# Kernel tuning notes

Measured on AMD Instinct MI355X. Metric: run time of the kernel, lower is better.

## Reference

```python
import jax, jax.numpy as jnp
import numpy as np

N = 40000      # nodes
E = 640000     # edges (avg degree 16)
F = 128        # in_feats
OUT = 128      # out_feats


def setup_inputs() -> dict:
    key = jax.random.key(0)
    ks = jax.random.split(key, 8)
    feat = jax.random.normal(ks[0], (N, F), dtype=jnp.float32)
    src = jax.random.randint(ks[1], (E,), 0, N, dtype=jnp.int32)
    dst = jnp.sort(jax.random.randint(ks[2], (E,), 0, N, dtype=jnp.int32))
    # AttentionAGG: fc1 (2F -> F), fc2 (F -> 1); fc_layer (2F -> OUT)
    s1 = 1.0 / np.sqrt(2 * F)
    s2 = 1.0 / np.sqrt(F)
    w1 = jax.random.normal(ks[3], (2 * F, F), dtype=jnp.float32) * s1
    b1 = jnp.zeros((F,), dtype=jnp.float32)
    w2 = jax.random.normal(ks[4], (F, 1), dtype=jnp.float32) * s2
    b2 = jnp.zeros((1,), dtype=jnp.float32)
    wf = jax.random.normal(ks[5], (2 * F, OUT), dtype=jnp.float32) * s1
    bf = jnp.zeros((OUT,), dtype=jnp.float32)
    return {"feat": feat, "src": src, "dst": dst,
            "w1": w1, "b1": b1, "w2": w2, "b2": b2, "wf": wf, "bf": bf}


def reference(feat, src, dst, w1, b1, w2, b2, wf, bf):
    f = feat.shape[1]
    n = feat.shape[0]
    # fc1(concat(h_dst, m_src)) == h_dst @ w1[:F] + h_src @ w1[F:]  (edge_weight is None)
    proj_dst = feat @ w1[:f]          # [N, F]
    proj_src = feat @ w1[f:]          # [N, F]
    pre = jnp.tanh(proj_dst[dst] + proj_src[src] + b1)   # [E, F]
    scores = (pre @ w2)[:, 0] + b2[0]                    # [E]
    # softmax over the ragged incoming-edge set of each dst node
    smax = jax.ops.segment_max(scores, dst, num_segments=n, indices_are_sorted=True)
    ex = jnp.exp(scores - jax.lax.stop_gradient(smax)[dst])
    den = jax.ops.segment_sum(ex, dst, num_segments=n, indices_are_sorted=True)
    att = ex / den[dst]                                  # [E]
    # weighted segment-sum of messages (m_e = feat[src]); zero-degree nodes get 0
    neigh = jax.ops.segment_sum(att[:, None] * feat[src], dst,
                                num_segments=n, indices_are_sorted=True)  # [N, F]
    # fc_layer(concat(h_self, neigh))
    rst = feat @ wf[:f] + neigh @ wf[f:] + bf            # [N, OUT]
    return rst
```

## Files before the change

### kernel.cpp

```cpp
#include <hip/hip_runtime.h>
#include <math.h>

#define F 128
#define OUT 128

typedef unsigned short ushort_t;
typedef __attribute__((ext_vector_type(8))) short bfrag;
typedef __attribute__((ext_vector_type(4))) float ffrag;

__device__ __forceinline__ float bf_lo(unsigned int u) {
    return __uint_as_float(u << 16);
}
__device__ __forceinline__ float bf_hi(unsigned int u) {
    return __uint_as_float(u & 0xffff0000u);
}
__device__ __forceinline__ ushort_t f2bf(float f) {
    unsigned int x = __float_as_uint(f);
    unsigned int r = x + 0x7fffu + ((x >> 16) & 1u);
    return (ushort_t)(r >> 16);
}
__device__ __forceinline__ unsigned pk2(float lo, float hi) {
    return (unsigned)f2bf(lo) | ((unsigned)f2bf(hi) << 16);
}

#define DPP_ADD(x, ctrl) \
    ((x) + __int_as_float(__builtin_amdgcn_update_dpp( \
        0, __float_as_int(x), (ctrl), 0xf, 0xf, true)))

__global__ __launch_bounds__(256) void prep_kernel(
    const float* __restrict__ feat, const float* __restrict__ w1,
    const float* __restrict__ wf, const int* __restrict__ dst,
    ushort_t* __restrict__ abig, ushort_t* __restrict__ srcpack,
    ushort_t* __restrict__ btp, ushort_t* __restrict__ btf,
    int* __restrict__ row_ptr, int n, int e, int nb0, int nb1, int nb2)
{
    const int b = blockIdx.x, t = threadIdx.x;
    if (b < nb0) {
        int i = b * 256 + t;
        if (i >= n * 16) return;
        int row = i >> 4, c = (i & 15) * 8;
        float4 a = *(const float4*)(feat + (size_t)row * F + c);
        float4 bb = *(const float4*)(feat + (size_t)row * F + c + 4);
        unsigned p0 = pk2(a.x, a.y), p1 = pk2(a.z, a.w);
        unsigned p2 = pk2(bb.x, bb.y), p3 = pk2(bb.z, bb.w);
        *(uint4*)(abig + (size_t)row * 256 + c) = make_uint4(p0, p1, p2, p3);
        *(uint2*)(srcpack + (size_t)row * 256 + c * 2 + 4) = make_uint2(p0, p1);
        *(uint2*)(srcpack + (size_t)row * 256 + c * 2 + 12) = make_uint2(p2, p3);
    } else if (b < nb0 + nb1) {
        int idx = (b - nb0) * 256 + t;
        int j = idx >> 7, k = idx & 127;
        float v = (j < F) ? w1[(size_t)k * F + j]
                          : w1[(size_t)(F + k) * F + (j - F)];
        btp[idx] = f2bf(v);
    } else if (b < nb0 + nb1 + nb2) {
        int idx = (b - nb0 - nb1) * 256 + t;
        int j = idx >> 8, k = idx & 255;
        btf[idx] = f2bf(wf[(size_t)k * F + j]);
    } else {
        int i = (b - nb0 - nb1 - nb2) * 256 + t;
        if (i >= e) return;
        int d = dst[i];
        int prev = (i == 0) ? -1 : dst[i - 1];
        for (int v = prev + 1; v <= d; ++v) row_ptr[v] = i;
        if (i == e - 1) {
            for (int v = d + 1; v <= n; ++v) row_ptr[v] = e;
        }
    }
}

#define PST 136
__global__ __launch_bounds__(256) void proj_gemm_kernel(
    const ushort_t* __restrict__ abig, const ushort_t* __restrict__ btp,
    const float* __restrict__ b1, ushort_t* __restrict__ e_dst,
    ushort_t* __restrict__ srcpack, int n)
{
    __shared__ ushort_t As[64 * PST];
    __shared__ ushort_t Ep[4][16 * 80];
    const int t = threadIdx.x;
    const int wv = t >> 6, lane = t & 63;
    const int lm = lane & 15, quad = lane >> 4;
    const int row0 = blockIdx.x * 64, col0 = wv * 64;

#pragma unroll
    for (int k = 0; k < 4; ++k) {
        int l = k * 256 + t;
        int r = l >> 4, ch = l & 15;
        uint4 d = make_uint4(0, 0, 0, 0);
        if (row0 + r < n) d = *(const uint4*)(abig + (size_t)(row0 + r) * 256 + ch * 8);
        *(uint4*)(As + r * PST + ch * 8) = d;
    }
    __syncthreads();

    bfrag bfr[4][4];
#pragma unroll
    for (int ks = 0; ks < 4; ++ks)
#pragma unroll
        for (int ni = 0; ni < 4; ++ni)
            bfr[ks][ni] = *(const bfrag*)(btp + (size_t)(col0 + ni * 16 + lm) * 128
                                          + ks * 32 + quad * 8);

    ffrag acc[4][4];
#pragma unroll
    for (int mi = 0; mi < 4; ++mi)
#pragma unroll
        for (int ni = 0; ni < 4; ++ni) acc[mi][ni] = (ffrag){0.f, 0.f, 0.f, 0.f};

#pragma unroll
    for (int ks = 0; ks < 4; ++ks)
#pragma unroll
        for (int mi = 0; mi < 4; ++mi) {
            bfrag af = *(const bfrag*)(As + (mi * 16 + lm) * PST + ks * 32 + quad * 8);
#pragma unroll
            for (int ni = 0; ni < 4; ++ni)
                acc[mi][ni] = __builtin_amdgcn_mfma_f32_16x16x32_bf16(
                    af, bfr[ks][ni], acc[mi][ni], 0, 0, 0);
        }

    float bias[4];
#pragma unroll
    for (int ni = 0; ni < 4; ++ni)
        bias[ni] = (col0 < F) ? b1[col0 + ni * 16 + lm] : 0.f;

#pragma unroll
    for (int mi = 0; mi < 4; ++mi) {
#pragma unroll
        for (int ni = 0; ni < 4; ++ni)
#pragma unroll
            for (int r = 0; r < 4; ++r)
                Ep[wv][(quad * 4 + r) * 80 + ni * 16 + lm] =
                    f2bf(__expf(2.f * (acc[mi][ni][r] + bias[ni])));
#pragma unroll
        for (int ps = 0; ps < 2; ++ps) {
            int rl = ps * 8 + (lane >> 3), co = (lane & 7) * 8;
            uint4 vv = *(const uint4*)(&Ep[wv][rl * 80 + co]);
            int grow = row0 + mi * 16 + rl;
            if (grow < n) {
                if (col0 < F) {
                    *(uint4*)(e_dst + (size_t)grow * F + col0 + co) = vv;
                } else {
                    int f0 = col0 - F + co;
                    *(uint2*)(srcpack + (size_t)grow * 256 + f0 * 2) =
                        make_uint2(vv.x, vv.y);
                    *(uint2*)(srcpack + (size_t)grow * 256 + f0 * 2 + 8) =
                        make_uint2(vv.z, vv.w);
                }
            }
        }
    }
}

__global__ __launch_bounds__(256) void fused_kernel(
    const ushort_t* __restrict__ e_dst, const ushort_t* __restrict__ srcpack,
    const int* __restrict__ src, const int* __restrict__ row_ptr,
    const float* __restrict__ w2, ushort_t* __restrict__ abig, int n, int nhw)
{
    const int hw0 = (int)((blockIdx.x * 256u + threadIdx.x) >> 5);
    const int fl = threadIdx.x & 31;

    const float4 wv4 = ((const float4*)w2)[fl];
    const float w0 = wv4.x, w1_ = wv4.y, w2_ = wv4.z, w3_ = wv4.w;
    float sw = w0 + w1_ + w2_ + w3_;
    float aw = fabsf(w0) + fabsf(w1_) + fabsf(w2_) + fabsf(w3_);
#pragma unroll
    for (int off = 16; off; off >>= 1) {
        sw += __shfl_xor(sw, off, 64);
        aw += __shfl_xor(aw, off, 64);
    }
    const float K = sw - aw;
    const float L2E = 1.4426950408889634f;
    const float K2 = K * L2E;

    const uint4* __restrict__ sp = (const uint4*)srcpack + fl;

    for (int v = hw0; v < n; v += nhw) {
        const int begin = row_ptr[v], end = row_ptr[v + 1];

        const uint2 ud = *(const uint2*)(e_dst + (size_t)v * F + fl * 4);
        const float ea0 = bf_lo(ud.x), ea1 = bf_hi(ud.x);
        const float ea2 = bf_lo(ud.y), ea3 = bf_hi(ud.y);

        float s = 0.f, a0 = 0.f, a1 = 0.f, a2 = 0.f, a3 = 0.f;

        int ee = begin;
        for (; ee + 4 <= end; ee += 4) {
            uint4 u[4];
#pragma unroll
            for (int q = 0; q < 4; ++q) {
                const int sq = src[ee + q];
                u[q] = sp[(size_t)sq * 32];
            }
            float p[4];
#pragma unroll
            for (int q = 0; q < 4; ++q) {
                float A = fmaf(ea0, bf_lo(u[q].x), 1.f);
                float B = fmaf(ea1, bf_hi(u[q].x), 1.f);
                float C = fmaf(ea2, bf_lo(u[q].y), 1.f);
                float D = fmaf(ea3, bf_hi(u[q].y), 1.f);
                float nAB = fmaf(w0, B, w1_ * A);
                float nCD = fmaf(w2_, D, w3_ * C);
                float rAB = __builtin_amdgcn_rcpf(A * B);
                float rCD = __builtin_amdgcn_rcpf(C * D);
                p[q] = fmaf(nAB, rAB, nCD * rCD);
            }
#pragma unroll
            for (int q = 0; q < 4; ++q) {
                p[q] = DPP_ADD(p[q], 0x121);
                p[q] = DPP_ADD(p[q], 0x122);
                p[q] = DPP_ADD(p[q], 0x124);
                p[q] = DPP_ADD(p[q], 0x128);
                p[q] += __shfl_xor(p[q], 16, 64);
            }
            float g[4];
#pragma unroll
            for (int q = 0; q < 4; ++q)
                g[q] = exp2f(fmaf(-2.f * L2E, p[q], K2));
            s += (g[0] + g[1]) + (g[2] + g[3]);
#pragma unroll
            for (int q = 0; q < 4; ++q) {
                a0 = fmaf(g[q], bf_lo(u[q].z), a0);
                a1 = fmaf(g[q], bf_hi(u[q].z), a1);
                a2 = fmaf(g[q], bf_lo(u[q].w), a2);
                a3 = fmaf(g[q], bf_hi(u[q].w), a3);
            }
        }
        for (; ee < end; ++ee) {
            const int s0 = src[ee];
            const uint4 u0 = sp[(size_t)s0 * 32];
            float A = fmaf(ea0, bf_lo(u0.x), 1.f);
            float B = fmaf(ea1, bf_hi(u0.x), 1.f);
            float C = fmaf(ea2, bf_lo(u0.y), 1.f);
            float D = fmaf(ea3, bf_hi(u0.y), 1.f);
            float nAB = fmaf(w0, B, w1_ * A);
            float nCD = fmaf(w2_, D, w3_ * C);
            float rAB = __builtin_amdgcn_rcpf(A * B);
            float rCD = __builtin_amdgcn_rcpf(C * D);
            float p0 = fmaf(nAB, rAB, nCD * rCD);
            p0 = DPP_ADD(p0, 0x121);
            p0 = DPP_ADD(p0, 0x122);
            p0 = DPP_ADD(p0, 0x124);
            p0 = DPP_ADD(p0, 0x128);
            p0 += __shfl_xor(p0, 16, 64);
            const float g0 = exp2f(fmaf(-2.f * L2E, p0, K2));
            s += g0;
            a0 = fmaf(g0, bf_lo(u0.z), a0);
            a1 = fmaf(g0, bf_hi(u0.z), a1);
            a2 = fmaf(g0, bf_lo(u0.w), a2);
            a3 = fmaf(g0, bf_hi(u0.w), a3);
        }

        const float inv = (end > begin) ? 1.f / s : 0.f;
        ushort4 o = make_ushort4(f2bf(a0 * inv), f2bf(a1 * inv),
                                 f2bf(a2 * inv), f2bf(a3 * inv));
        *(ushort4*)(abig + (size_t)v * 256 + 128 + fl * 4) = o;
    }
}

#define OST 280
__global__ __launch_bounds__(256) void out_gemm_kernel(
    const ushort_t* __restrict__ abig, const ushort_t* __restrict__ btf,
    const float* __restrict__ bfv, float* __restrict__ out, int n)
{
    __shared__ ushort_t As[64 * OST];
    const int t = threadIdx.x;
    const int wv = t >> 6, lane = t & 63;
    const int lm = lane & 15, quad = lane >> 4;
    const int row0 = blockIdx.x * 64, col0 = wv * 32;

#pragma unroll
    for (int k = 0; k < 8; ++k) {
        int l = k * 256 + t;
        int r = l >> 5, ch = l & 31;
        uint4 d = make_uint4(0, 0, 0, 0);
        if (row0 + r < n) d = *(const uint4*)(abig + (size_t)(row0 + r) * 256 + ch * 8);
        *(uint4*)(As + r * OST + ch * 8) = d;
    }
    __syncthreads();

    bfrag bfr[8][2];
#pragma unroll
    for (int ks = 0; ks < 8; ++ks)
#pragma unroll
        for (int ni = 0; ni < 2; ++ni)
            bfr[ks][ni] = *(const bfrag*)(btf + (size_t)(col0 + ni * 16 + lm) * 256
                                          + ks * 32 + quad * 8);

    ffrag acc[4][2];
#pragma unroll
    for (int mi = 0; mi < 4; ++mi)
#pragma unroll
        for (int ni = 0; ni < 2; ++ni) acc[mi][ni] = (ffrag){0.f, 0.f, 0.f, 0.f};

#pragma unroll
    for (int ks = 0; ks < 8; ++ks)
#pragma unroll
        for (int mi = 0; mi < 4; ++mi) {
            bfrag af = *(const bfrag*)(As + (mi * 16 + lm) * OST + ks * 32 + quad * 8);
#pragma unroll
            for (int ni = 0; ni < 2; ++ni)
                acc[mi][ni] = __builtin_amdgcn_mfma_f32_16x16x32_bf16(
                    af, bfr[ks][ni], acc[mi][ni], 0, 0, 0);
        }

#pragma unroll
    for (int ni = 0; ni < 2; ++ni) {
        const int j = col0 + ni * 16 + lm;
        const float bb = bfv[j];
#pragma unroll
        for (int mi = 0; mi < 4; ++mi)
#pragma unroll
            for (int r = 0; r < 4; ++r) {
                int grow = row0 + mi * 16 + quad * 4 + r;
                if (grow < n) out[(size_t)grow * OUT + j] = acc[mi][ni][r] + bb;
            }
    }
}

extern "C" void kernel_launch(void* const* d_in, const int* in_sizes, int n_in,
                              void* d_out, int out_size, void* d_ws, size_t ws_size,
                              hipStream_t stream)
{
    const float* feat = (const float*)d_in[0];
    const int*   src  = (const int*)d_in[1];
    const int*   dst  = (const int*)d_in[2];
    const float* w1   = (const float*)d_in[3];
    const float* b1   = (const float*)d_in[4];
    const float* w2   = (const float*)d_in[5];
    const float* b2   = (const float*)d_in[6];  (void)b2;
    const float* wf   = (const float*)d_in[7];
    const float* bfv  = (const float*)d_in[8];
    float* out = (float*)d_out;

    const int n = in_sizes[0] / F;
    const int e = in_sizes[1];

    ushort_t* abig    = (ushort_t*)d_ws;
    ushort_t* e_dst   = abig + (size_t)n * 256;
    ushort_t* srcpack = e_dst + (size_t)n * 128;
    ushort_t* btp     = srcpack + (size_t)n * 256;
    ushort_t* btf     = btp + 32768;
    int* row_ptr      = (int*)(btf + 32768);

    const int nb0 = (n * 16 + 255) / 256;
    const int nb1 = 128, nb2 = 128;
    const int nb3 = (e + 255) / 256;

    const int fblocks = 1250;
    const int nhw = fblocks * 8;

    prep_kernel<<<nb0 + nb1 + nb2 + nb3, 256, 0, stream>>>(
        feat, w1, wf, dst, abig, srcpack, btp, btf, row_ptr, n, e, nb0, nb1, nb2);
    proj_gemm_kernel<<<(n + 63) / 64, 256, 0, stream>>>(
        abig, btp, b1, e_dst, srcpack, n);
    fused_kernel<<<fblocks, 256, 0, stream>>>(
        e_dst, srcpack, src, row_ptr, w2, abig, n, nhw);
    out_gemm_kernel<<<(n + 63) / 64, 256, 0, stream>>>(abig, btf, bfv, out, n);
}
```

Measured before the change: 170.8 us.

## Store gathered source features as FP8 and batch edge index loads via shuffles

The per-node gather record changes from interleaved bf16 (512 B) to 256 B of bf16 projection plus 128 B of FP8 raw features (384 B per row). This cuts the bytes moved by the random gather in the edge-aggregation kernel. The fused kernel now loads up to 32 src indices at once and broadcasts them with shuffles, and it uses one half-wave per node instead of a grid-stride loop. The FP8 rounding of the message features lowers accuracy of the aggregated neighbour sum and may threaten tolerance.

```diff
diff --git a/kernel.cpp b/kernel.cpp
--- a/kernel.cpp
+++ b/kernel.cpp
@@ -7,6 +7,7 @@
 typedef unsigned short ushort_t;
 typedef __attribute__((ext_vector_type(8))) short bfrag;
 typedef __attribute__((ext_vector_type(4))) float ffrag;
+typedef __attribute__((ext_vector_type(2))) float fx2;
 
 __device__ __forceinline__ float bf_lo(unsigned int u) {
     return __uint_as_float(u << 16);
@@ -26,6 +27,7 @@
 #define DPP_ADD(x, ctrl) \
     ((x) + __int_as_float(__builtin_amdgcn_update_dpp( \
         0, __float_as_int(x), (ctrl), 0xf, 0xf, true)))
+
 
 __global__ __launch_bounds__(256) void prep_kernel(
     const float* __restrict__ feat, const float* __restrict__ w1,
@@ -44,8 +46,11 @@
         unsigned p0 = pk2(a.x, a.y), p1 = pk2(a.z, a.w);
         unsigned p2 = pk2(bb.x, bb.y), p3 = pk2(bb.z, bb.w);
         *(uint4*)(abig + (size_t)row * 256 + c) = make_uint4(p0, p1, p2, p3);
-        *(uint2*)(srcpack + (size_t)row * 256 + c * 2 + 4) = make_uint2(p0, p1);
-        *(uint2*)(srcpack + (size_t)row * 256 + c * 2 + 12) = make_uint2(p2, p3);
+        unsigned w01 = (unsigned)__builtin_amdgcn_cvt_pk_fp8_f32(a.x, a.y, 0, false);
+        w01 = (unsigned)__builtin_amdgcn_cvt_pk_fp8_f32(a.z, a.w, (int)w01, true);
+        unsigned w23 = (unsigned)__builtin_amdgcn_cvt_pk_fp8_f32(bb.x, bb.y, 0, false);
+        w23 = (unsigned)__builtin_amdgcn_cvt_pk_fp8_f32(bb.z, bb.w, (int)w23, true);
+        *(uint2*)((char*)srcpack + (size_t)row * 384 + 256 + c) = make_uint2(w01, w23);
     } else if (b < nb0 + nb1) {
         int idx = (b - nb0) * 256 + t;
         int j = idx >> 7, k = idx & 127;
@@ -139,10 +144,7 @@
                     *(uint4*)(e_dst + (size_t)grow * F + col0 + co) = vv;
                 } else {
                     int f0 = col0 - F + co;
-                    *(uint2*)(srcpack + (size_t)grow * 256 + f0 * 2) =
-                        make_uint2(vv.x, vv.y);
-                    *(uint2*)(srcpack + (size_t)grow * 256 + f0 * 2 + 8) =
-                        make_uint2(vv.z, vv.w);
+                    *(uint4*)((char*)srcpack + (size_t)grow * 384 + (size_t)f0 * 2) = vv;
                 }
             }
         }
@@ -152,10 +154,11 @@
 __global__ __launch_bounds__(256) void fused_kernel(
     const ushort_t* __restrict__ e_dst, const ushort_t* __restrict__ srcpack,
     const int* __restrict__ src, const int* __restrict__ row_ptr,
-    const float* __restrict__ w2, ushort_t* __restrict__ abig, int n, int nhw)
-{
-    const int hw0 = (int)((blockIdx.x * 256u + threadIdx.x) >> 5);
+    const float* __restrict__ w2, ushort_t* __restrict__ abig, int n)
+{
+    const int v = (int)((blockIdx.x * 256u + threadIdx.x) >> 5);
     const int fl = threadIdx.x & 31;
+    const int sbase = threadIdx.x & 32;
 
     const float4 wv4 = ((const float4*)w2)[fl];
     const float w0 = wv4.x, w1_ = wv4.y, w2_ = wv4.z, w3_ = wv4.w;
@@ -170,24 +173,30 @@
     const float L2E = 1.4426950408889634f;
     const float K2 = K * L2E;
 
-    const uint4* __restrict__ sp = (const uint4*)srcpack + fl;
-
-    for (int v = hw0; v < n; v += nhw) {
-        const int begin = row_ptr[v], end = row_ptr[v + 1];
-
-        const uint2 ud = *(const uint2*)(e_dst + (size_t)v * F + fl * 4);
-        const float ea0 = bf_lo(ud.x), ea1 = bf_hi(ud.x);
-        const float ea2 = bf_lo(ud.y), ea3 = bf_hi(ud.y);
-
-        float s = 0.f, a0 = 0.f, a1 = 0.f, a2 = 0.f, a3 = 0.f;
-
-        int ee = begin;
-        for (; ee + 4 <= end; ee += 4) {
-            uint4 u[4];
+    if (v >= n) return;
+    const int begin = row_ptr[v], end = row_ptr[v + 1];
+
+    const uint2 ud = *(const uint2*)(e_dst + (size_t)v * F + fl * 4);
+    const float ea0 = bf_lo(ud.x), ea1 = bf_hi(ud.x);
+    const float ea2 = bf_lo(ud.y), ea3 = bf_hi(ud.y);
+
+    const char* __restrict__ spb = (const char*)srcpack;
+
+    float s = 0.f, a0 = 0.f, a1 = 0.f, a2 = 0.f, a3 = 0.f;
+
+    for (int cb = begin; cb < end; cb += 32) {
+        const int clen = min(32, end - cb);
+        const int sv = (fl < clen) ? src[cb + fl] : 0;
+        int jj = 0;
+        for (; jj + 4 <= clen; jj += 4) {
+            uint2 u[4];
+            unsigned vf[4];
 #pragma unroll
             for (int q = 0; q < 4; ++q) {
-                const int sq = src[ee + q];
-                u[q] = sp[(size_t)sq * 32];
+                const int sq = __shfl(sv, sbase + jj + q, 64);
+                const char* rb = spb + (size_t)sq * 384;
+                u[q] = ((const uint2*)rb)[fl];
+                vf[q] = ((const unsigned*)(rb + 256))[fl];
             }
             float p[4];
 #pragma unroll
@@ -217,15 +226,19 @@
             s += (g[0] + g[1]) + (g[2] + g[3]);
 #pragma unroll
             for (int q = 0; q < 4; ++q) {
-                a0 = fmaf(g[q], bf_lo(u[q].z), a0);
-                a1 = fmaf(g[q], bf_hi(u[q].z), a1);
-                a2 = fmaf(g[q], bf_lo(u[q].w), a2);
-                a3 = fmaf(g[q], bf_hi(u[q].w), a3);
-            }
-        }
-        for (; ee < end; ++ee) {
-            const int s0 = src[ee];
-            const uint4 u0 = sp[(size_t)s0 * 32];
+                fx2 lo = __builtin_amdgcn_cvt_pk_f32_fp8((int)vf[q], false);
+                fx2 hi = __builtin_amdgcn_cvt_pk_f32_fp8((int)vf[q], true);
+                a0 = fmaf(g[q], lo[0], a0);
+                a1 = fmaf(g[q], lo[1], a1);
+                a2 = fmaf(g[q], hi[0], a2);
+                a3 = fmaf(g[q], hi[1], a3);
+            }
+        }
+        for (; jj < clen; ++jj) {
+            const int s0 = __shfl(sv, sbase + jj, 64);
+            const char* rb = spb + (size_t)s0 * 384;
+            const uint2 u0 = ((const uint2*)rb)[fl];
+            const unsigned vf0 = ((const unsigned*)(rb + 256))[fl];
             float A = fmaf(ea0, bf_lo(u0.x), 1.f);
             float B = fmaf(ea1, bf_hi(u0.x), 1.f);
             float C = fmaf(ea2, bf_lo(u0.y), 1.f);
@@ -242,17 +255,19 @@
             p0 += __shfl_xor(p0, 16, 64);
             const float g0 = exp2f(fmaf(-2.f * L2E, p0, K2));
             s += g0;
-            a0 = fmaf(g0, bf_lo(u0.z), a0);
-            a1 = fmaf(g0, bf_hi(u0.z), a1);
-            a2 = fmaf(g0, bf_lo(u0.w), a2);
-            a3 = fmaf(g0, bf_hi(u0.w), a3);
-        }
-
-        const float inv = (end > begin) ? 1.f / s : 0.f;
-        ushort4 o = make_ushort4(f2bf(a0 * inv), f2bf(a1 * inv),
-                                 f2bf(a2 * inv), f2bf(a3 * inv));
-        *(ushort4*)(abig + (size_t)v * 256 + 128 + fl * 4) = o;
-    }
+            fx2 lo = __builtin_amdgcn_cvt_pk_f32_fp8((int)vf0, false);
+            fx2 hi = __builtin_amdgcn_cvt_pk_f32_fp8((int)vf0, true);
+            a0 = fmaf(g0, lo[0], a0);
+            a1 = fmaf(g0, lo[1], a1);
+            a2 = fmaf(g0, hi[0], a2);
+            a3 = fmaf(g0, hi[1], a3);
+        }
+    }
+
+    const float inv = (end > begin) ? 1.f / s : 0.f;
+    ushort4 o = make_ushort4(f2bf(a0 * inv), f2bf(a1 * inv),
+                             f2bf(a2 * inv), f2bf(a3 * inv));
+    *(ushort4*)(abig + (size_t)v * 256 + 128 + fl * 4) = o;
 }
 
 #define OST 280
@@ -336,22 +351,19 @@
     ushort_t* abig    = (ushort_t*)d_ws;
     ushort_t* e_dst   = abig + (size_t)n * 256;
     ushort_t* srcpack = e_dst + (size_t)n * 128;
-    ushort_t* btp     = srcpack + (size_t)n * 256;
+    ushort_t* btp     = srcpack + (size_t)n * 192;
     ushort_t* btf     = btp + 32768;
     int* row_ptr      = (int*)(btf + 32768);
 
     const int nb0 = (n * 16 + 255) / 256;
     const int nb1 = 128, nb2 = 128;
     const int nb3 = (e + 255) / 256;
-
-    const int fblocks = 1250;
-    const int nhw = fblocks * 8;
 
     prep_kernel<<<nb0 + nb1 + nb2 + nb3, 256, 0, stream>>>(
         feat, w1, wf, dst, abig, srcpack, btp, btf, row_ptr, n, e, nb0, nb1, nb2);
     proj_gemm_kernel<<<(n + 63) / 64, 256, 0, stream>>>(
         abig, btp, b1, e_dst, srcpack, n);
-    fused_kernel<<<fblocks, 256, 0, stream>>>(
-        e_dst, srcpack, src, row_ptr, w2, abig, n, nhw);
+    fused_kernel<<<(n + 7) / 8, 256, 0, stream>>>(
+        e_dst, srcpack, src, row_ptr, w2, abig, n);
     out_gemm_kernel<<<(n + 63) / 64, 256, 0, stream>>>(abig, btf, bfv, out, n);
 }
```

After: 153.3 us. -10.3%, faster.
